# Kernel optimization log

Hardware: AMD Instinct MI355X
Metric: run time of the kernel (lower is better)

## Reference

```python
import jax, jax.numpy as jnp
import numpy as np

N = 8192; E = 131072; K = 20; IN_DIM = 3; HID = 256; N_CLASSES = 32


def setup_inputs():
    key = jax.random.key(0)
    ks = jax.random.split(key, 16)

    def w(k, shape):
        lim = 1.0 / np.sqrt(shape[0])
        return jax.random.uniform(k, shape, jnp.float32, -lim, lim)

    f32 = jnp.float32
    return {
        "features": jax.random.normal(ks[0], (N, IN_DIM), f32),
        "src": jax.random.randint(ks[1], (E,), 0, N, jnp.int32),
        "dst": jax.random.randint(ks[2], (E,), 0, N, jnp.int32),
        # GraphConv params
        "Wc1": w(ks[3], (IN_DIM, HID)), "bc1": jnp.zeros((HID,), f32),
        "Wc2": w(ks[4], (HID, HID)), "bc2": jnp.zeros((HID,), f32),
        "Wc3": w(ks[5], (64, N_CLASSES)), "bc3": jnp.zeros((N_CLASSES,), f32),
        # DynamicEdgeConv 1 MLP: [2*256 -> 256 -> 256], Linear+BN+ReLU each
        "W11": w(ks[6], (2 * HID, 256)), "b11": jnp.zeros((256,), f32), "g11": jnp.ones((256,), f32), "be11": jnp.zeros((256,), f32),
        "W12": w(ks[7], (256, 256)), "b12": jnp.zeros((256,), f32), "g12": jnp.ones((256,), f32), "be12": jnp.zeros((256,), f32),
        # DynamicEdgeConv 2 MLP: [2*256 -> 64 -> 64]
        "W21": w(ks[8], (2 * 256, 64)), "b21": jnp.zeros((64,), f32), "g21": jnp.ones((64,), f32), "be21": jnp.zeros((64,), f32),
        "W22": w(ks[9], (64, 64)), "b22": jnp.zeros((64,), f32), "g22": jnp.ones((64,), f32), "be22": jnp.zeros((64,), f32),
    }


def reference(features, src, dst, Wc1, bc1, Wc2, bc2, Wc3, bc3,
              W11, b11, g11, be11, W12, b12, g12, be12,
              W21, b21, g21, be21, W22, b22, g22, be22):
    n = features.shape[0]
    ones_e = jnp.ones(src.shape[0], features.dtype)
    # DGL GraphConv norm='both': deg clamped to min 1
    dout = jnp.clip(jax.ops.segment_sum(ones_e, src, num_segments=n), 1.0) ** -0.5
    din = jnp.clip(jax.ops.segment_sum(ones_e, dst, num_segments=n), 1.0) ** -0.5

    def gconv(x, W, b, act):
        agg = jax.ops.segment_sum((x * dout[:, None])[src], dst, num_segments=n)
        r = (agg * din[:, None]) @ W + b
        return jax.nn.relu(r) if act else r

    def bn(x, g, b):  # BatchNorm1d in training mode over all edge rows
        mu = jnp.mean(x, axis=(0, 1), keepdims=True)
        var = jnp.mean(jnp.square(x - mu), axis=(0, 1), keepdims=True)
        return (x - mu) * jax.lax.rsqrt(var + 1e-5) * g + b

    def edge_conv(x, layers):
        # dynamic kNN graph on current features (self included, dist 0)
        sq = jnp.sum(x * x, axis=-1)
        d = sq[:, None] + sq[None, :] - 2.0 * (x @ x.T)  # [N,N]
        idx = jax.lax.top_k(-d, K)[1]                    # [N,K]
        xi = x[:, None, :]
        e = jnp.concatenate([jnp.broadcast_to(xi, (n, K, x.shape[-1])), x[idx] - xi], axis=-1)  # [N,K,2F]
        for W, b, g, be in layers:
            e = jax.nn.relu(bn(e @ W + b, g, be))
        return jnp.max(e, axis=1)  # max aggregation over neighbors

    h = gconv(features, Wc1, bc1, True)                                   # [N,256]
    h = edge_conv(h, [(W11, b11, g11, be11), (W12, b12, g12, be12)])      # [N,256]
    h = gconv(h, Wc2, bc2, True)                                          # [N,256]
    h = edge_conv(h, [(W21, b21, g21, be21), (W22, b22, g22, be22)])      # [N,64]
    return gconv(h, Wc3, bc3, False)                                      # [N,32]
```

## Files before the change

kernel.cpp:

```cpp
#include <hip/hip_runtime.h>

#define NN 8192
#define NE 131072
#define KNN 20
#define CH 4096
#define GBM 128
#define GBN 128
#define GBK 64

typedef __attribute__((ext_vector_type(4))) float f32x4;
typedef __attribute__((ext_vector_type(8))) __bf16 bf16x8;

__global__ void k_zero(float* p, int n){
  int i = blockIdx.x*256 + threadIdx.x;
  if (i < n) p[i] = 0.f;
}
__global__ void k_zero_i(int* p, int n){
  int i = blockIdx.x*256 + threadIdx.x;
  if (i < n) p[i] = 0;
}

__device__ __forceinline__ unsigned short f2bf(float x){
  unsigned u = __float_as_uint(x);
  unsigned r = (u + 0x7fff + ((u >> 16) & 1)) >> 16;
  return (unsigned short)r;
}
__device__ __forceinline__ float bf2f(unsigned short h){
  return __uint_as_float((unsigned)h << 16);
}
__device__ __forceinline__ void gload16(const void* g, void* l){
  __builtin_amdgcn_global_load_lds(
      (const __attribute__((address_space(1))) void*)g,
      (__attribute__((address_space(3))) void*)l, 16, 0, 0);
}

__global__ void k_count(const int* __restrict__ src, const int* __restrict__ dst,
                        int* cs, int* cd){
  int e = blockIdx.x*256 + threadIdx.x;
  if (e < NE){ atomicAdd(&cs[src[e]], 1); atomicAdd(&cd[dst[e]], 1); }
}
__global__ void k_deg(const int* cs, const int* cd, float* dout, float* din){
  int i = blockIdx.x*256 + threadIdx.x;
  if (i < NN){
    dout[i] = rsqrtf((float)max(cs[i], 1));
    din[i]  = rsqrtf((float)max(cd[i], 1));
  }
}
__global__ void k_scan(const int* __restrict__ cnt, int* __restrict__ off){
  __shared__ int sh[256];
  __shared__ int carry;
  int tid = threadIdx.x;
  if (tid == 0) carry = 0;
  __syncthreads();
  for (int base = 0; base < NN; base += 256){
    int v = cnt[base + tid];
    int x = v;
    sh[tid] = x; __syncthreads();
    for (int o = 1; o < 256; o <<= 1){
      int y = (tid >= o) ? sh[tid - o] : 0;
      __syncthreads();
      x += y; sh[tid] = x;
      __syncthreads();
    }
    off[base + tid] = carry + x - v;
    __syncthreads();
    if (tid == 255){
      carry += x;
      if (base + 256 == NN) off[NN] = carry;
    }
    __syncthreads();
  }
}
__global__ void k_fill(const int* __restrict__ src, const int* __restrict__ dst,
                       const int* __restrict__ roff, int* cursor, int* csr){
  int e = blockIdx.x*256 + threadIdx.x;
  if (e < NE){
    int d = dst[e];
    int p = atomicAdd(&cursor[d], 1);
    csr[roff[d] + p] = src[e];
  }
}

__global__ void k_gconv1(const float* __restrict__ feat, const int* __restrict__ roff,
                         const int* __restrict__ csr, const float* __restrict__ dout,
                         const float* __restrict__ din, const float* __restrict__ Wc1,
                         const float* __restrict__ bc1, float* __restrict__ h1){
  int wid = threadIdx.x >> 6, lane = threadIdx.x & 63;
  int i = blockIdx.x*4 + wid;
  float a0=0.f, a1=0.f, a2=0.f;
  int beg = roff[i], end = roff[i+1];
  for (int t = beg + lane; t < end; t += 64){
    int s = csr[t]; float w = dout[s];
    a0 += feat[s*3+0]*w; a1 += feat[s*3+1]*w; a2 += feat[s*3+2]*w;
  }
  for (int m = 32; m; m >>= 1){
    a0 += __shfl_xor(a0, m); a1 += __shfl_xor(a1, m); a2 += __shfl_xor(a2, m);
  }
  float dn = din[i];
  a0 *= dn; a1 *= dn; a2 *= dn;
  for (int c = lane; c < 256; c += 64){
    float r = a0*Wc1[c] + a1*Wc1[256+c] + a2*Wc1[512+c] + bc1[c];
    h1[(size_t)i*256 + c] = fmaxf(r, 0.f);
  }
}

__global__ void k_sq(const float* __restrict__ X, float* __restrict__ sq){
  int wid = threadIdx.x >> 6, lane = threadIdx.x & 63;
  int i = blockIdx.x*4 + wid;
  float4 v = *(const float4*)&X[(size_t)i*256 + lane*4];
  float s = v.x*v.x + v.y*v.y + v.z*v.z + v.w*v.w;
  for (int m = 32; m; m >>= 1) s += __shfl_xor(s, m);
  if (lane == 0) sq[i] = s;
}

__global__ void k_split(const float* __restrict__ X, unsigned short* __restrict__ xcat){
  int row = blockIdx.x, c = threadIdx.x;
  float x = X[(size_t)row*256 + c];
  unsigned short h = f2bf(x);
  unsigned short lo = f2bf(x - bf2f(h));
  xcat[(size_t)row*512 + c] = h;
  xcat[(size_t)row*512 + 256 + c] = lo;
}

__global__ void k_wsplit(const float* __restrict__ W, unsigned short* __restrict__ Whi,
                         unsigned short* __restrict__ Wlo){
  int k = blockIdx.x, n = threadIdx.x;
  float x = W[(size_t)k*256 + n];
  unsigned short h = f2bf(x);
  Whi[(size_t)n*256 + k] = h;
  Wlo[(size_t)n*256 + k] = f2bf(x - bf2f(h));
}
__global__ void k_wsplit64(const float* __restrict__ W, unsigned short* __restrict__ Whi,
                           unsigned short* __restrict__ Wlo){
  int k = blockIdx.x, n = threadIdx.x;
  float x = W[(size_t)k*64 + n];
  unsigned short h = f2bf(x);
  Whi[(size_t)n*64 + k] = h;
  Wlo[(size_t)n*64 + k] = f2bf(x - bf2f(h));
}

__global__ __launch_bounds__(256)
void k_gram_mfma(const unsigned short* __restrict__ Xcat,
                 float* __restrict__ G, int r0){
  __shared__ unsigned short sA[GBM*GBK];
  __shared__ unsigned short sB[GBM*GBK];
  int tid = threadIdx.x;
  int lw = tid >> 6, l = tid & 63;
  int rbl = blockIdx.y*GBM;
  int rb = r0 + rbl;
  int cb = blockIdx.x*GBN;

  int srow = l >> 3;
  int scol = (l & 7) ^ srow;
  const unsigned short* srcA[4];
  const unsigned short* srcB[4];
  char* dstA[4]; char* dstB[4];
  #pragma unroll
  for (int i = 0; i < 4; i++){
    int c = lw*4 + i;
    int row = c*8 + srow;
    srcA[i] = Xcat + (size_t)(rb + row)*512 + scol*8;
    srcB[i] = Xcat + (size_t)(cb + row)*512 + scol*8;
    dstA[i] = (char*)sA + c*1024;
    dstB[i] = (char*)sB + c*1024;
  }

  int wm = lw >> 1, wn = lw & 1;
  int fm = l & 15, kg = l >> 4;
  unsigned offA[4][2], offB[4][2];
  #pragma unroll
  for (int mf = 0; mf < 4; mf++){
    int rowa = wm*64 + mf*16 + fm;
    int rowb = wn*64 + mf*16 + fm;
    #pragma unroll
    for (int ks = 0; ks < 2; ks++){
      offA[mf][ks] = rowa*128 + (((unsigned)(ks*4 + kg) ^ (rowa & 7)))*16;
      offB[mf][ks] = rowb*128 + (((unsigned)(ks*4 + kg) ^ (rowb & 7)))*16;
    }
  }

  f32x4 acc[4][4];
  #pragma unroll
  for (int m = 0; m < 4; m++)
    #pragma unroll
    for (int n = 0; n < 4; n++) acc[m][n] = (f32x4){0.f,0.f,0.f,0.f};

  #pragma unroll
  for (int s = 0; s < 12; s++){
    int sec = s >> 2;
    int inner = (s & 3)*64;
    int cbA = (sec == 1 ? 256 : 0) + inner;
    int cbB = (sec == 2 ? 256 : 0) + inner;
    #pragma unroll
    for (int i = 0; i < 4; i++){
      gload16(srcA[i] + cbA, dstA[i]);
      gload16(srcB[i] + cbB, dstB[i]);
    }
    __syncthreads();
    #pragma unroll
    for (int ks = 0; ks < 2; ks++){
      bf16x8 a[4], b[4];
      #pragma unroll
      for (int mf = 0; mf < 4; mf++) a[mf] = *(const bf16x8*)((const char*)sA + offA[mf][ks]);
      #pragma unroll
      for (int nf = 0; nf < 4; nf++) b[nf] = *(const bf16x8*)((const char*)sB + offB[nf][ks]);
      #pragma unroll
      for (int mf = 0; mf < 4; mf++)
        #pragma unroll
        for (int nf = 0; nf < 4; nf++)
          acc[mf][nf] = __builtin_amdgcn_mfma_f32_16x16x32_bf16(a[mf], b[nf], acc[mf][nf], 0, 0, 0);
    }
    __syncthreads();
  }

  #pragma unroll
  for (int mf = 0; mf < 4; mf++){
    int orow = rbl + wm*64 + mf*16 + kg*4;
    #pragma unroll
    for (int nf = 0; nf < 4; nf++){
      int ocol = cb + wn*64 + nf*16 + fm;
      #pragma unroll
      for (int r = 0; r < 4; r++)
        G[(size_t)(orow + r)*NN + ocol] = acc[mf][nf][r];
    }
  }
}

__global__ __launch_bounds__(256)
void k_topk(const float* __restrict__ G, const float* __restrict__ sq,
            int r0, int* __restrict__ idxo){
  __shared__ float lsq[NN];
  int tid = threadIdx.x;
  for (int t = tid; t < NN/4; t += 256)
    ((float4*)lsq)[t] = ((const float4*)sq)[t];
  __syncthreads();

  int wid = tid >> 6, lane = tid & 63;
  int rl = blockIdx.x*4 + wid;
  int gr = r0 + rl;
  const float4* row4 = (const float4*)(G + (size_t)rl*NN);
  const float4* lsq4 = (const float4*)lsq;
  float sqr = lsq[gr];

  float kd0=INFINITY,kd1=INFINITY,kd2=INFINITY,kd3=INFINITY,kd4=INFINITY,
        kd5=INFINITY,kd6=INFINITY,kd7=INFINITY,kd8=INFINITY,kd9=INFINITY,
        kd10=INFINITY,kd11=INFINITY,kd12=INFINITY,kd13=INFINITY,kd14=INFINITY,
        kd15=INFINITY,kd16=INFINITY,kd17=INFINITY,kd18=INFINITY,kd19=INFINITY;
  int ki0=0x7fffffff,ki1=0x7fffffff,ki2=0x7fffffff,ki3=0x7fffffff,ki4=0x7fffffff,
      ki5=0x7fffffff,ki6=0x7fffffff,ki7=0x7fffffff,ki8=0x7fffffff,ki9=0x7fffffff,
      ki10=0x7fffffff,ki11=0x7fffffff,ki12=0x7fffffff,ki13=0x7fffffff,ki14=0x7fffffff,
      ki15=0x7fffffff,ki16=0x7fffffff,ki17=0x7fffffff,ki18=0x7fffffff,ki19=0x7fffffff;

#define ST(U) { bool sw = nk < kd##U; float tv = kd##U; int tq = ki##U; \
      if (sw){ kd##U = nk; ki##U = ni; nk = tv; ni = tq; } }
#define INSE(kc, jc) { if ((kc) < kd19){ float nk = (kc); int ni = (jc); \
      ST(0) ST(1) ST(2) ST(3) ST(4) ST(5) ST(6) ST(7) ST(8) ST(9) \
      ST(10) ST(11) ST(12) ST(13) ST(14) ST(15) ST(16) ST(17) ST(18) ST(19) } }

  float4 gc = row4[lane];
  float4 sc = lsq4[lane];
  #pragma unroll 1
  for (int o = 0; o < 32; o++){
    float4 g = gc, s = sc;
    if (o < 31){
      gc = row4[lane + (o+1)*64];
      sc = lsq4[lane + (o+1)*64];
    }
    int jb = (lane + o*64)*4;
    float k0 = (sqr + s.x) - 2.f*g.x;
    float k1 = (sqr + s.y) - 2.f*g.y;
    float k2 = (sqr + s.z) - 2.f*g.z;
    float k3 = (sqr + s.w) - 2.f*g.w;
    float t19 = kd19;
    float mn = fminf(fminf(k0,k1), fminf(k2,k3));
    if (__any(mn < t19)){
      INSE(k0, jb+0);
      INSE(k1, jb+1);
      INSE(k2, jb+2);
      INSE(k3, jb+3);
    }
  }
#undef INSE
#undef ST

#define MV(A,B) { kd##A = kd##B; ki##A = ki##B; }
  #pragma unroll 1
  for (int r = 0; r < KNN; r++){
    float bv = kd0; int bi = ki0;
    #pragma unroll
    for (int mm = 32; mm; mm >>= 1){
      float ov = __shfl_xor(bv, mm); int oi = __shfl_xor(bi, mm);
      if (ov < bv || (ov == bv && oi < bi)){ bv = ov; bi = oi; }
    }
    if (ki0 == bi){
      MV(0,1) MV(1,2) MV(2,3) MV(3,4) MV(4,5) MV(5,6) MV(6,7) MV(7,8) MV(8,9) MV(9,10)
      MV(10,11) MV(11,12) MV(12,13) MV(13,14) MV(14,15) MV(15,16) MV(16,17) MV(17,18) MV(18,19)
      kd19 = INFINITY; ki19 = 0x7fffffff;
    }
    if (lane == 0) idxo[(size_t)gr*KNN + r] = bi;
  }
#undef MV
}

__global__ void k_wd(const float* __restrict__ W, float* __restrict__ Wd, int rows, int M){
  int t = blockIdx.x*256 + threadIdx.x;
  if (t < rows*M) Wd[t] = W[t] - W[rows*M + t];
}

__global__ __launch_bounds__(256)
void k_mm(const float* __restrict__ A, const float* __restrict__ B,
          const float* __restrict__ bias, float* __restrict__ Cout,
          int n, int Kd, int M, int relu){
  __shared__ float la[16][68], lb[16][68];
  int tid = threadIdx.x;
  int rb = blockIdx.y*64, cb = blockIdx.x*64;
  int lr = tid >> 2, lq = (tid & 3)*4;
  int ty = tid >> 4, tx = tid & 15;
  float acc[4][4] = {};
  for (int k0 = 0; k0 < Kd; k0 += 16){
    __syncthreads();
    #pragma unroll
    for (int u = 0; u < 4; u++){
      int k = k0 + lq + u;
      la[lq+u][lr] = (k < Kd) ? A[(size_t)(rb+lr)*Kd + k] : 0.f;
    }
    int kk = tid >> 4; int cc = (tid & 15)*4;
    #pragma unroll
    for (int u = 0; u < 4; u++){
      int c = cb + cc + u; int k = k0 + kk;
      lb[kk][cc+u] = (k < Kd && c < M) ? B[(size_t)k*M + c] : 0.f;
    }
    __syncthreads();
    #pragma unroll
    for (int k = 0; k < 16; k++){
      float4 a = *(const float4*)&la[k][ty*4];
      float4 b = *(const float4*)&lb[k][tx*4];
      float avv[4] = {a.x,a.y,a.z,a.w}, bvv[4] = {b.x,b.y,b.z,b.w};
      #pragma unroll
      for (int u = 0; u < 4; u++)
        #pragma unroll
        for (int v = 0; v < 4; v++) acc[u][v] += avv[u]*bvv[v];
    }
  }
  #pragma unroll
  for (int u = 0; u < 4; u++){
    int r = rb + ty*4 + u;
    #pragma unroll
    for (int v = 0; v < 4; v++){
      int c = cb + tx*4 + v;
      if (c < M){
        float x = acc[u][v] + (bias ? bias[c] : 0.f);
        if (relu) x = fmaxf(x, 0.f);
        Cout[(size_t)r*M + c] = x;
      }
    }
  }
}

template<int C>
__global__ __launch_bounds__(256)
void k_stats1(const float* __restrict__ A, const float* __restrict__ P,
              const int* __restrict__ idx, float* __restrict__ ssum, float* __restrict__ ssq){
  __shared__ int si[128], sj[128];
  int tid = threadIdx.x;
  int s0 = blockIdx.x*128;
  if (tid < 128){ si[tid] = (s0 + tid)/KNN; sj[tid] = idx[s0 + tid]; }
  __syncthreads();
  constexpr int MPAR = 256/C;
  int tc = tid % C, sr = tid / C;
  float s = 0.f, q = 0.f;
  for (int m = sr; m < 128; m += MPAR){
    float v = A[(size_t)si[m]*C + tc] + P[(size_t)sj[m]*C + tc];
    s += v; q += v*v;
  }
  if constexpr (MPAR > 1){
    __shared__ float rs[256], rq[256];
    rs[tid] = s; rq[tid] = q; __syncthreads();
    if (sr == 0){
      for (int u = 1; u < MPAR; u++){ s += rs[u*C + tc]; q += rq[u*C + tc]; }
    }
  }
  if (sr == 0){ atomicAdd(&ssum[tc], s); atomicAdd(&ssq[tc], q); }
}

__global__ void k_bn_final(const float* __restrict__ ssum, const float* __restrict__ ssq,
                           const float* __restrict__ g, const float* __restrict__ be,
                           float* __restrict__ sb, float* __restrict__ tb, int C, float invn){
  int c = threadIdx.x;
  if (c < C){
    float mu = ssum[c]*invn;
    float var = fmaxf(ssq[c]*invn - mu*mu, 0.f);
    float s = g[c]*rsqrtf(var + 1e-5f);
    sb[c] = s; tb[c] = be[c] - mu*s;
  }
}

__global__ __launch_bounds__(256, 2)
void k_edge_mfma(const float* __restrict__ A, const float* __restrict__ P,
                 const int* __restrict__ idx, const float* __restrict__ sb,
                 const float* __restrict__ tb, const unsigned short* __restrict__ Wthi,
                 const unsigned short* __restrict__ Wtlo, const float* __restrict__ bias,
                 float* __restrict__ out, float* __restrict__ ssum, float* __restrict__ ssq){
  __shared__ unsigned short ehi[64*256];
  __shared__ unsigned short elo[64*256];
  __shared__ int sj[64];
  int tid = threadIdx.x;
  int lw = tid >> 6, l = tid & 63;
  int s0 = blockIdx.x*64;
  if (tid < 64) sj[tid] = idx[s0 + tid];
  float sbc = sb[tid], tbc = tb[tid];
  __syncthreads();

  #pragma unroll 1
  for (int g = 0; g < 8; g++){
    float va[8];
    #pragma unroll
    for (int u = 0; u < 8; u++){
      int it = g*8 + u;
      int i = (s0 + it)/KNN;
      int j = sj[it];
      va[u] = A[(size_t)i*256 + tid] + P[(size_t)j*256 + tid];
    }
    #pragma unroll
    for (int u = 0; u < 8; u++){
      int it = g*8 + u;
      float v = fmaxf(va[u]*sbc + tbc, 0.f);
      unsigned short h = f2bf(v);
      unsigned short lo = f2bf(v - bf2f(h));
      unsigned off = (unsigned)it*512 + (((unsigned)tid*2) ^ (((unsigned)it & 7) << 4));
      *(unsigned short*)((char*)ehi + off) = h;
      *(unsigned short*)((char*)elo + off) = lo;
    }
  }
  __syncthreads();

  int fm = l & 15, kg = l >> 4;
  const unsigned short* bhi[4];
  const unsigned short* blo[4];
  float bz[4];
  #pragma unroll
  for (int nf = 0; nf < 4; nf++){
    int col = lw*64 + nf*16 + fm;
    bhi[nf] = Wthi + (size_t)col*256 + kg*8;
    blo[nf] = Wtlo + (size_t)col*256 + kg*8;
    bz[nf] = bias[col];
  }

  f32x4 acc[4][4];
  #pragma unroll
  for (int m = 0; m < 4; m++)
    #pragma unroll
    for (int n = 0; n < 4; n++) acc[m][n] = (f32x4){0.f,0.f,0.f,0.f};

  #pragma unroll 1
  for (int sec = 0; sec < 3; sec++){
    const char* abase = (sec == 1) ? (const char*)elo : (const char*)ehi;
    int bsec = (sec == 2);
    #pragma unroll 1
    for (int st = 0; st < 8; st++){
      int g = st*4 + kg;
      bf16x8 a[4], b[4];
      #pragma unroll
      for (int mf = 0; mf < 4; mf++){
        int row = mf*16 + fm;
        a[mf] = *(const bf16x8*)(abase + row*512 + ((unsigned)(g ^ (row & 7)))*16);
      }
      #pragma unroll
      for (int nf = 0; nf < 4; nf++){
        const unsigned short* bp = bsec ? blo[nf] : bhi[nf];
        b[nf] = *(const bf16x8*)(bp + st*32);
      }
      #pragma unroll
      for (int mf = 0; mf < 4; mf++)
        #pragma unroll
        for (int nf = 0; nf < 4; nf++)
          acc[mf][nf] = __builtin_amdgcn_mfma_f32_16x16x32_bf16(a[mf], b[nf], acc[mf][nf], 0, 0, 0);
    }
  }

  float s4[4], q4[4];
  #pragma unroll
  for (int nf = 0; nf < 4; nf++){ s4[nf] = 0.f; q4[nf] = 0.f; }
  #pragma unroll
  for (int mf = 0; mf < 4; mf++){
    #pragma unroll
    for (int nf = 0; nf < 4; nf++){
      int col = lw*64 + nf*16 + fm;
      #pragma unroll
      for (int r = 0; r < 4; r++){
        int row = s0 + mf*16 + kg*4 + r;
        float v = acc[mf][nf][r] + bz[nf];
        out[(size_t)row*256 + col] = v;
        s4[nf] += v; q4[nf] += v*v;
      }
    }
  }
  #pragma unroll
  for (int nf = 0; nf < 4; nf++){
    s4[nf] += __shfl_xor(s4[nf], 16); q4[nf] += __shfl_xor(q4[nf], 16);
    s4[nf] += __shfl_xor(s4[nf], 32); q4[nf] += __shfl_xor(q4[nf], 32);
  }
  if (kg == 0){
    #pragma unroll
    for (int nf = 0; nf < 4; nf++){
      int col = lw*64 + nf*16 + fm;
      atomicAdd(&ssum[col], s4[nf]);
      atomicAdd(&ssq[col], q4[nf]);
    }
  }
}

__global__ __launch_bounds__(256, 2)
void k_edge_mfma64(const float* __restrict__ A, const float* __restrict__ P,
                   const int* __restrict__ idx, const float* __restrict__ sb,
                   const float* __restrict__ tb, const unsigned short* __restrict__ Wthi,
                   const unsigned short* __restrict__ Wtlo, const float* __restrict__ bias,
                   float* __restrict__ out, float* __restrict__ ssum, float* __restrict__ ssq){
  __shared__ unsigned short ehi[128*64];
  __shared__ unsigned short elo[128*64];
  __shared__ int sj[128];
  int tid = threadIdx.x;
  int lw = tid >> 6, l = tid & 63;
  int s0 = blockIdx.x*128;
  if (tid < 128) sj[tid] = idx[s0 + tid];
  int col0 = tid & 63, rgrp = tid >> 6;
  float sbc = sb[col0], tbc = tb[col0];
  __syncthreads();

  #pragma unroll 1
  for (int g = 0; g < 4; g++){
    float va[8];
    #pragma unroll
    for (int u = 0; u < 8; u++){
      int it = (g*8 + u)*4 + rgrp;
      int i = (s0 + it)/KNN;
      int j = sj[it];
      va[u] = A[(size_t)i*64 + col0] + P[(size_t)j*64 + col0];
    }
    #pragma unroll
    for (int u = 0; u < 8; u++){
      int it = (g*8 + u)*4 + rgrp;
      float v = fmaxf(va[u]*sbc + tbc, 0.f);
      unsigned short h = f2bf(v);
      unsigned short lo = f2bf(v - bf2f(h));
      unsigned off = (unsigned)it*128 + (((unsigned)col0*2) ^ (((unsigned)it & 7) << 4));
      *(unsigned short*)((char*)ehi + off) = h;
      *(unsigned short*)((char*)elo + off) = lo;
    }
  }
  __syncthreads();

  int wm = lw >> 1, wn = lw & 1;
  int fm = l & 15, kg = l >> 4;
  const unsigned short* bhi[2];
  const unsigned short* blo[2];
  float bz[2];
  #pragma unroll
  for (int nf = 0; nf < 2; nf++){
    int col = wn*32 + nf*16 + fm;
    bhi[nf] = Wthi + (size_t)col*64 + kg*8;
    blo[nf] = Wtlo + (size_t)col*64 + kg*8;
    bz[nf] = bias[col];
  }

  f32x4 acc[4][2];
  #pragma unroll
  for (int m = 0; m < 4; m++)
    #pragma unroll
    for (int n = 0; n < 2; n++) acc[m][n] = (f32x4){0.f,0.f,0.f,0.f};

  #pragma unroll 1
  for (int sec = 0; sec < 3; sec++){
    const char* abase = (sec == 1) ? (const char*)elo : (const char*)ehi;
    int bsec = (sec == 2);
    #pragma unroll
    for (int ks = 0; ks < 2; ks++){
      int g = ks*4 + kg;
      bf16x8 a[4], b[2];
      #pragma unroll
      for (int mf = 0; mf < 4; mf++){
        int row = wm*64 + mf*16 + fm;
        a[mf] = *(const bf16x8*)(abase + row*128 + ((unsigned)(g ^ (row & 7)))*16);
      }
      #pragma unroll
      for (int nf = 0; nf < 2; nf++){
        const unsigned short* bp = bsec ? blo[nf] : bhi[nf];
        b[nf] = *(const bf16x8*)(bp + ks*32);
      }
      #pragma unroll
      for (int mf = 0; mf < 4; mf++)
        #pragma unroll
        for (int nf = 0; nf < 2; nf++)
          acc[mf][nf] = __builtin_amdgcn_mfma_f32_16x16x32_bf16(a[mf], b[nf], acc[mf][nf], 0, 0, 0);
    }
  }

  float s2[2], q2[2];
  #pragma unroll
  for (int nf = 0; nf < 2; nf++){ s2[nf] = 0.f; q2[nf] = 0.f; }
  #pragma unroll
  for (int mf = 0; mf < 4; mf++){
    #pragma unroll
    for (int nf = 0; nf < 2; nf++){
      int col = wn*32 + nf*16 + fm;
      #pragma unroll
      for (int r = 0; r < 4; r++){
        int row = s0 + wm*64 + mf*16 + kg*4 + r;
        float v = acc[mf][nf][r] + bz[nf];
        out[(size_t)row*64 + col] = v;
        s2[nf] += v; q2[nf] += v*v;
      }
    }
  }
  #pragma unroll
  for (int nf = 0; nf < 2; nf++){
    s2[nf] += __shfl_xor(s2[nf], 16); q2[nf] += __shfl_xor(q2[nf], 16);
    s2[nf] += __shfl_xor(s2[nf], 32); q2[nf] += __shfl_xor(q2[nf], 32);
  }
  if (kg == 0){
    #pragma unroll
    for (int nf = 0; nf < 2; nf++){
      int col = wn*32 + nf*16 + fm;
      atomicAdd(&ssum[col], s2[nf]);
      atomicAdd(&ssq[col], q2[nf]);
    }
  }
}

template<int C>
__global__ void k_maxpool(const float* __restrict__ X, const float* __restrict__ sb,
                          const float* __restrict__ tb, float* __restrict__ H){
  constexpr int NPB = 256/C;
  int node = blockIdx.x*NPB + threadIdx.x / C;
  int c = threadIdx.x % C;
  float s = sb[c], t = tb[c];
  float mx = 0.f;
  for (int k = 0; k < KNN; k++){
    float v = X[(size_t)(node*KNN + k)*C + c]*s + t;
    mx = fmaxf(mx, v);
  }
  H[(size_t)node*C + c] = mx;
}

template<int C>
__global__ void k_agg(const float* __restrict__ X, const int* __restrict__ roff,
                      const int* __restrict__ csr, const float* __restrict__ dout,
                      const float* __restrict__ din, float* __restrict__ XA){
  int i = blockIdx.x; int c = threadIdx.x;
  float acc = 0.f;
  int b = roff[i], e = roff[i+1];
  for (int t = b; t < e; t++){
    int s = csr[t];
    acc += X[(size_t)s*C + c]*dout[s];
  }
  XA[(size_t)i*C + c] = acc*din[i];
}

extern "C" void kernel_launch(void* const* d_in, const int* in_sizes, int n_in,
                              void* d_out, int out_size, void* d_ws, size_t ws_size,
                              hipStream_t stream){
  const float* feat = (const float*)d_in[0];
  const int*   src  = (const int*)d_in[1];
  const int*   dst  = (const int*)d_in[2];
  const float* Wc1  = (const float*)d_in[3];
  const float* bc1  = (const float*)d_in[4];
  const float* Wc2  = (const float*)d_in[5];
  const float* bc2  = (const float*)d_in[6];
  const float* Wc3  = (const float*)d_in[7];
  const float* bc3  = (const float*)d_in[8];
  const float* W11  = (const float*)d_in[9];
  const float* b11  = (const float*)d_in[10];
  const float* g11  = (const float*)d_in[11];
  const float* be11 = (const float*)d_in[12];
  const float* W12  = (const float*)d_in[13];
  const float* b12  = (const float*)d_in[14];
  const float* g12  = (const float*)d_in[15];
  const float* be12 = (const float*)d_in[16];
  const float* W21  = (const float*)d_in[17];
  const float* b21  = (const float*)d_in[18];
  const float* g21  = (const float*)d_in[19];
  const float* be21 = (const float*)d_in[20];
  const float* W22  = (const float*)d_in[21];
  const float* b22  = (const float*)d_in[22];
  const float* g22  = (const float*)d_in[23];
  const float* be22 = (const float*)d_in[24];
  float* out = (float*)d_out;

  char* w = (char*)d_ws; size_t off = 0;
  auto alloc = [&](size_t bytes)->void*{
    void* p = w + off;
    off += bytes; off = (off + 255) & ~(size_t)255;
    return p;
  };
  int* cnt_s  = (int*)alloc(NN*4);
  int* cnt_d  = (int*)alloc(NN*4);
  int* roff   = (int*)alloc((NN+1)*4);
  int* cursor = (int*)alloc(NN*4);
  int* csr    = (int*)alloc(NE*4);
  int* idx    = (int*)alloc((size_t)NN*KNN*4);
  float* dout = (float*)alloc(NN*4);
  float* din  = (float*)alloc(NN*4);
  float* sqv  = (float*)alloc(NN*4);
  float* h1   = (float*)alloc((size_t)NN*256*4);
  float* h2   = (float*)alloc((size_t)NN*256*4);
  float* h3   = (float*)alloc((size_t)NN*256*4);
  float* h4   = (float*)alloc((size_t)NN*64*4);
  float* xa   = (float*)alloc((size_t)NN*256*4);
  float* Abuf = (float*)alloc((size_t)NN*256*4);
  float* Pbuf = (float*)alloc((size_t)NN*256*4);
  float* Wd   = (float*)alloc(256*256*4);
  float* ssum = (float*)alloc(256*4);
  float* ssq  = (float*)alloc(256*4);
  float* sbn  = (float*)alloc(256*4);
  float* tbn  = (float*)alloc(256*4);
  unsigned short* wthi = (unsigned short*)alloc(256*256*2);
  unsigned short* wtlo = (unsigned short*)alloc(256*256*2);
  unsigned short* w64hi = (unsigned short*)alloc(64*64*2);
  unsigned short* w64lo = (unsigned short*)alloc(64*64*2);
  float* out2 = (float*)alloc((size_t)NN*KNN*256*4);
  float* gram = out2;
  unsigned short* xcat = (unsigned short*)(out2 + (size_t)CH*NN);
  (void)ws_size; (void)n_in; (void)in_sizes; (void)out_size;

  const float invn = 1.0f / (float)(NN*KNN);

  k_zero_i<<<32, 256, 0, stream>>>(cnt_s, NN);
  k_zero_i<<<32, 256, 0, stream>>>(cnt_d, NN);
  k_zero_i<<<32, 256, 0, stream>>>(cursor, NN);
  k_count<<<NE/256, 256, 0, stream>>>(src, dst, cnt_s, cnt_d);
  k_deg<<<32, 256, 0, stream>>>(cnt_s, cnt_d, dout, din);
  k_scan<<<1, 256, 0, stream>>>(cnt_d, roff);
  k_fill<<<NE/256, 256, 0, stream>>>(src, dst, roff, cursor, csr);

  k_gconv1<<<NN/4, 256, 0, stream>>>(feat, roff, csr, dout, din, Wc1, bc1, h1);

  k_sq<<<NN/4, 256, 0, stream>>>(h1, sqv);
  k_split<<<NN, 256, 0, stream>>>(h1, xcat);
  for (int r0 = 0; r0 < NN; r0 += CH){
    k_gram_mfma<<<dim3(NN/GBN, CH/GBM), 256, 0, stream>>>(xcat, gram, r0);
    k_topk<<<CH/4, 256, 0, stream>>>(gram, sqv, r0, idx);
  }
  k_wd<<<256, 256, 0, stream>>>(W11, Wd, 256, 256);
  k_wsplit<<<256, 256, 0, stream>>>(W12, wthi, wtlo);
  k_mm<<<dim3(4, NN/64), 256, 0, stream>>>(h1, Wd, b11, Abuf, NN, 256, 256, 0);
  k_mm<<<dim3(4, NN/64), 256, 0, stream>>>(h1, W11 + 256*256, nullptr, Pbuf, NN, 256, 256, 0);
  k_zero<<<2, 256, 0, stream>>>(ssum, 256); k_zero<<<2, 256, 0, stream>>>(ssq, 256);
  k_stats1<256><<<NN*KNN/128, 256, 0, stream>>>(Abuf, Pbuf, idx, ssum, ssq);
  k_bn_final<<<1, 256, 0, stream>>>(ssum, ssq, g11, be11, sbn, tbn, 256, invn);
  k_zero<<<2, 256, 0, stream>>>(ssum, 256); k_zero<<<2, 256, 0, stream>>>(ssq, 256);
  k_edge_mfma<<<NN*KNN/64, 256, 0, stream>>>(Abuf, Pbuf, idx, sbn, tbn, wthi, wtlo, b12, out2, ssum, ssq);
  k_bn_final<<<1, 256, 0, stream>>>(ssum, ssq, g12, be12, sbn, tbn, 256, invn);
  k_maxpool<256><<<NN, 256, 0, stream>>>(out2, sbn, tbn, h2);

  k_agg<256><<<NN, 256, 0, stream>>>(h2, roff, csr, dout, din, xa);
  k_mm<<<dim3(4, NN/64), 256, 0, stream>>>(xa, Wc2, bc2, h3, NN, 256, 256, 1);

  k_sq<<<NN/4, 256, 0, stream>>>(h3, sqv);
  k_split<<<NN, 256, 0, stream>>>(h3, xcat);
  for (int r0 = 0; r0 < NN; r0 += CH){
    k_gram_mfma<<<dim3(NN/GBN, CH/GBM), 256, 0, stream>>>(xcat, gram, r0);
    k_topk<<<CH/4, 256, 0, stream>>>(gram, sqv, r0, idx);
  }
  k_wd<<<64, 256, 0, stream>>>(W21, Wd, 256, 64);
  k_wsplit64<<<64, 64, 0, stream>>>(W22, w64hi, w64lo);
  k_mm<<<dim3(1, NN/64), 256, 0, stream>>>(h3, Wd, b21, Abuf, NN, 256, 64, 0);
  k_mm<<<dim3(1, NN/64), 256, 0, stream>>>(h3, W21 + 256*64, nullptr, Pbuf, NN, 256, 64, 0);
  k_zero<<<2, 256, 0, stream>>>(ssum, 256); k_zero<<<2, 256, 0, stream>>>(ssq, 256);
  k_stats1<64><<<NN*KNN/128, 256, 0, stream>>>(Abuf, Pbuf, idx, ssum, ssq);
  k_bn_final<<<1, 256, 0, stream>>>(ssum, ssq, g21, be21, sbn, tbn, 64, invn);
  k_zero<<<2, 256, 0, stream>>>(ssum, 256); k_zero<<<2, 256, 0, stream>>>(ssq, 256);
  k_edge_mfma64<<<NN*KNN/128, 256, 0, stream>>>(Abuf, Pbuf, idx, sbn, tbn, w64hi, w64lo, b22, out2, ssum, ssq);
  k_bn_final<<<1, 256, 0, stream>>>(ssum, ssq, g22, be22, sbn, tbn, 64, invn);
  k_maxpool<64><<<NN/4, 256, 0, stream>>>(out2, sbn, tbn, h4);

  k_agg<64><<<NN, 64, 0, stream>>>(h4, roff, csr, dout, din, xa);
  k_mm<<<dim3(1, NN/64), 256, 0, stream>>>(xa, Wc3, bc3, out, NN, 64, 32, 0);
}
```

Before: 1.393 ms.

## Use split-bf16 MFMA for node GEMMs and shrink edge MFMA tile

Replaces the scalar fp32 tiled k_mm for the 256-wide node-level GEMMs (edge-conv layer-1 A/P projections and the GraphConv2 linear) with a new MFMA kernel. It reuses the hi/lo bf16 split activations (xcat) and split weights, using three bf16 passes to approximate fp32 accuracy. The edge MFMA kernel also halves its row tile from 64 to 32 edges per block and raises occupancy from 2 to 4 blocks. Each wave now covers 16 rows by 128 columns, trading more blocks and less A reuse for lower LDS and register use. This adds several extra weight-split and activation-split launches, and reuses xcat, which still holds the h1 split from the kNN stage.

New measurement: 1.789 ms. +28.5%, slower.

```diff
diff --git a/kernel.cpp b/kernel.cpp
--- a/kernel.cpp
+++ b/kernel.cpp
@@ -308,6 +308,61 @@
 }
 
 __global__ __launch_bounds__(256)
+void k_mm_mfma(const unsigned short* __restrict__ Xc, const unsigned short* __restrict__ Wthi,
+               const unsigned short* __restrict__ Wtlo, const float* __restrict__ bias,
+               float* __restrict__ C, int relu){
+  int tid = threadIdx.x;
+  int lw = tid >> 6, l = tid & 63;
+  int wm = lw >> 1, wn = lw & 1;
+  int fm = l & 15, kg = l >> 4;
+  int rb = blockIdx.x*32;
+
+  const unsigned short* aptr = Xc + (size_t)(rb + wm*16 + fm)*512 + kg*8;
+  const unsigned short* bhi[8];
+  const unsigned short* blo[8];
+  float bz[8];
+  #pragma unroll
+  for (int nf = 0; nf < 8; nf++){
+    int col = wn*128 + nf*16 + fm;
+    bhi[nf] = Wthi + (size_t)col*256 + kg*8;
+    blo[nf] = Wtlo + (size_t)col*256 + kg*8;
+    bz[nf] = bias ? bias[col] : 0.f;
+  }
+
+  f32x4 acc[8];
+  #pragma unroll
+  for (int n = 0; n < 8; n++) acc[n] = (f32x4){0.f,0.f,0.f,0.f};
+
+  #pragma unroll 1
+  for (int sec = 0; sec < 3; sec++){
+    int ka = (sec == 1) ? 256 : 0;
+    int bsec = (sec == 2);
+    #pragma unroll
+    for (int st = 0; st < 8; st++){
+      bf16x8 a = *(const bf16x8*)(aptr + ka + st*32);
+      #pragma unroll
+      for (int nf = 0; nf < 8; nf++){
+        const unsigned short* bp = bsec ? blo[nf] : bhi[nf];
+        bf16x8 b = *(const bf16x8*)(bp + st*32);
+        acc[nf] = __builtin_amdgcn_mfma_f32_16x16x32_bf16(a, b, acc[nf], 0, 0, 0);
+      }
+    }
+  }
+
+  #pragma unroll
+  for (int nf = 0; nf < 8; nf++){
+    int col = wn*128 + nf*16 + fm;
+    #pragma unroll
+    for (int r = 0; r < 4; r++){
+      int row = rb + wm*16 + kg*4 + r;
+      float v = acc[nf][r] + bz[nf];
+      if (relu) v = fmaxf(v, 0.f);
+      C[(size_t)row*256 + col] = v;
+    }
+  }
+}
+
+__global__ __launch_bounds__(256)
 void k_mm(const float* __restrict__ A, const float* __restrict__ B,
           const float* __restrict__ bias, float* __restrict__ Cout,
           int n, int Kd, int M, int relu){
@@ -395,24 +450,24 @@
   }
 }
 
-__global__ __launch_bounds__(256, 2)
+__global__ __launch_bounds__(256, 4)
 void k_edge_mfma(const float* __restrict__ A, const float* __restrict__ P,
                  const int* __restrict__ idx, const float* __restrict__ sb,
                  const float* __restrict__ tb, const unsigned short* __restrict__ Wthi,
                  const unsigned short* __restrict__ Wtlo, const float* __restrict__ bias,
                  float* __restrict__ out, float* __restrict__ ssum, float* __restrict__ ssq){
-  __shared__ unsigned short ehi[64*256];
-  __shared__ unsigned short elo[64*256];
-  __shared__ int sj[64];
+  __shared__ unsigned short ehi[32*256];
+  __shared__ unsigned short elo[32*256];
+  __shared__ int sj[32];
   int tid = threadIdx.x;
   int lw = tid >> 6, l = tid & 63;
-  int s0 = blockIdx.x*64;
-  if (tid < 64) sj[tid] = idx[s0 + tid];
+  int s0 = blockIdx.x*32;
+  if (tid < 32) sj[tid] = idx[s0 + tid];
   float sbc = sb[tid], tbc = tb[tid];
   __syncthreads();
 
   #pragma unroll 1
-  for (int g = 0; g < 8; g++){
+  for (int g = 0; g < 4; g++){
     float va[8];
     #pragma unroll
     for (int u = 0; u < 8; u++){
@@ -434,78 +489,58 @@
   }
   __syncthreads();
 
+  int wm = lw >> 1, wn = lw & 1;
   int fm = l & 15, kg = l >> 4;
-  const unsigned short* bhi[4];
-  const unsigned short* blo[4];
-  float bz[4];
-  #pragma unroll
-  for (int nf = 0; nf < 4; nf++){
-    int col = lw*64 + nf*16 + fm;
+  const unsigned short* bhi[8];
+  const unsigned short* blo[8];
+  float bz[8];
+  #pragma unroll
+  for (int nf = 0; nf < 8; nf++){
+    int col = wn*128 + nf*16 + fm;
     bhi[nf] = Wthi + (size_t)col*256 + kg*8;
     blo[nf] = Wtlo + (size_t)col*256 + kg*8;
     bz[nf] = bias[col];
   }
 
-  f32x4 acc[4][4];
-  #pragma unroll
-  for (int m = 0; m < 4; m++)
-    #pragma unroll
-    for (int n = 0; n < 4; n++) acc[m][n] = (f32x4){0.f,0.f,0.f,0.f};
-
+  f32x4 acc[8];
+  #pragma unroll
+  for (int n = 0; n < 8; n++) acc[n] = (f32x4){0.f,0.f,0.f,0.f};
+
+  int arow = wm*16 + fm;
+  unsigned abase_off = (unsigned)arow*512;
   #pragma unroll 1
   for (int sec = 0; sec < 3; sec++){
     const char* abase = (sec == 1) ? (const char*)elo : (const char*)ehi;
     int bsec = (sec == 2);
-    #pragma unroll 1
+    #pragma unroll
     for (int st = 0; st < 8; st++){
       int g = st*4 + kg;
-      bf16x8 a[4], b[4];
-      #pragma unroll
-      for (int mf = 0; mf < 4; mf++){
-        int row = mf*16 + fm;
-        a[mf] = *(const bf16x8*)(abase + row*512 + ((unsigned)(g ^ (row & 7)))*16);
+      bf16x8 a = *(const bf16x8*)(abase + abase_off + ((unsigned)(g ^ (arow & 7)))*16);
+      #pragma unroll
+      for (int nf = 0; nf < 8; nf++){
+        const unsigned short* bp = bsec ? blo[nf] : bhi[nf];
+        bf16x8 b = *(const bf16x8*)(bp + st*32);
+        acc[nf] = __builtin_amdgcn_mfma_f32_16x16x32_bf16(a, b, acc[nf], 0, 0, 0);
       }
-      #pragma unroll
-      for (int nf = 0; nf < 4; nf++){
-        const unsigned short* bp = bsec ? blo[nf] : bhi[nf];
-        b[nf] = *(const bf16x8*)(bp + st*32);
-      }
-      #pragma unroll
-      for (int mf = 0; mf < 4; mf++)
-        #pragma unroll
-        for (int nf = 0; nf < 4; nf++)
-          acc[mf][nf] = __builtin_amdgcn_mfma_f32_16x16x32_bf16(a[mf], b[nf], acc[mf][nf], 0, 0, 0);
-    }
-  }
-
-  float s4[4], q4[4];
-  #pragma unroll
-  for (int nf = 0; nf < 4; nf++){ s4[nf] = 0.f; q4[nf] = 0.f; }
-  #pragma unroll
-  for (int mf = 0; mf < 4; mf++){
-    #pragma unroll
-    for (int nf = 0; nf < 4; nf++){
-      int col = lw*64 + nf*16 + fm;
-      #pragma unroll
-      for (int r = 0; r < 4; r++){
-        int row = s0 + mf*16 + kg*4 + r;
-        float v = acc[mf][nf][r] + bz[nf];
-        out[(size_t)row*256 + col] = v;
-        s4[nf] += v; q4[nf] += v*v;
-      }
-    }
-  }
-  #pragma unroll
-  for (int nf = 0; nf < 4; nf++){
-    s4[nf] += __shfl_xor(s4[nf], 16); q4[nf] += __shfl_xor(q4[nf], 16);
-    s4[nf] += __shfl_xor(s4[nf], 32); q4[nf] += __shfl_xor(q4[nf], 32);
-  }
-  if (kg == 0){
-    #pragma unroll
-    for (int nf = 0; nf < 4; nf++){
-      int col = lw*64 + nf*16 + fm;
-      atomicAdd(&ssum[col], s4[nf]);
-      atomicAdd(&ssq[col], q4[nf]);
+    }
+  }
+
+  #pragma unroll
+  for (int nf = 0; nf < 8; nf++){
+    int col = wn*128 + nf*16 + fm;
+    float s4 = 0.f, q4 = 0.f;
+    #pragma unroll
+    for (int r = 0; r < 4; r++){
+      int row = s0 + wm*16 + kg*4 + r;
+      float v = acc[nf][r] + bz[nf];
+      out[(size_t)row*256 + col] = v;
+      s4 += v; q4 += v*v;
+    }
+    s4 += __shfl_xor(s4, 16); q4 += __shfl_xor(q4, 16);
+    s4 += __shfl_xor(s4, 32); q4 += __shfl_xor(q4, 32);
+    if (kg == 0){
+      atomicAdd(&ssum[col], s4);
+      atomicAdd(&ssq[col], q4);
     }
   }
 }
@@ -715,6 +750,12 @@
   float* tbn  = (float*)alloc(256*4);
   unsigned short* wthi = (unsigned short*)alloc(256*256*2);
   unsigned short* wtlo = (unsigned short*)alloc(256*256*2);
+  unsigned short* wdhi = (unsigned short*)alloc(256*256*2);
+  unsigned short* wdlo = (unsigned short*)alloc(256*256*2);
+  unsigned short* wbhi = (unsigned short*)alloc(256*256*2);
+  unsigned short* wblo = (unsigned short*)alloc(256*256*2);
+  unsigned short* wchi = (unsigned short*)alloc(256*256*2);
+  unsigned short* wclo = (unsigned short*)alloc(256*256*2);
   unsigned short* w64hi = (unsigned short*)alloc(64*64*2);
   unsigned short* w64lo = (unsigned short*)alloc(64*64*2);
   float* out2 = (float*)alloc((size_t)NN*KNN*256*4);
@@ -741,19 +782,23 @@
     k_topk<<<CH/4, 256, 0, stream>>>(gram, sqv, r0, idx);
   }
   k_wd<<<256, 256, 0, stream>>>(W11, Wd, 256, 256);
+  k_wsplit<<<256, 256, 0, stream>>>(Wd, wdhi, wdlo);
+  k_wsplit<<<256, 256, 0, stream>>>(W11 + 256*256, wbhi, wblo);
   k_wsplit<<<256, 256, 0, stream>>>(W12, wthi, wtlo);
-  k_mm<<<dim3(4, NN/64), 256, 0, stream>>>(h1, Wd, b11, Abuf, NN, 256, 256, 0);
-  k_mm<<<dim3(4, NN/64), 256, 0, stream>>>(h1, W11 + 256*256, nullptr, Pbuf, NN, 256, 256, 0);
+  k_mm_mfma<<<NN/32, 256, 0, stream>>>(xcat, wdhi, wdlo, b11, Abuf, 0);
+  k_mm_mfma<<<NN/32, 256, 0, stream>>>(xcat, wbhi, wblo, nullptr, Pbuf, 0);
   k_zero<<<2, 256, 0, stream>>>(ssum, 256); k_zero<<<2, 256, 0, stream>>>(ssq, 256);
   k_stats1<256><<<NN*KNN/128, 256, 0, stream>>>(Abuf, Pbuf, idx, ssum, ssq);
   k_bn_final<<<1, 256, 0, stream>>>(ssum, ssq, g11, be11, sbn, tbn, 256, invn);
   k_zero<<<2, 256, 0, stream>>>(ssum, 256); k_zero<<<2, 256, 0, stream>>>(ssq, 256);
-  k_edge_mfma<<<NN*KNN/64, 256, 0, stream>>>(Abuf, Pbuf, idx, sbn, tbn, wthi, wtlo, b12, out2, ssum, ssq);
+  k_edge_mfma<<<NN*KNN/32, 256, 0, stream>>>(Abuf, Pbuf, idx, sbn, tbn, wthi, wtlo, b12, out2, ssum, ssq);
   k_bn_final<<<1, 256, 0, stream>>>(ssum, ssq, g12, be12, sbn, tbn, 256, invn);
   k_maxpool<256><<<NN, 256, 0, stream>>>(out2, sbn, tbn, h2);
 
   k_agg<256><<<NN, 256, 0, stream>>>(h2, roff, csr, dout, din, xa);
-  k_mm<<<dim3(4, NN/64), 256, 0, stream>>>(xa, Wc2, bc2, h3, NN, 256, 256, 1);
+  k_split<<<NN, 256, 0, stream>>>(xa, xcat);
+  k_wsplit<<<256, 256, 0, stream>>>(Wc2, wchi, wclo);
+  k_mm_mfma<<<NN/32, 256, 0, stream>>>(xcat, wchi, wclo, bc2, h3, 1);
 
   k_sq<<<NN/4, 256, 0, stream>>>(h3, sqv);
   k_split<<<NN, 256, 0, stream>>>(h3, xcat);
```

## Fuse distance epilogue into gram kernel and move 256-wide linears to MFMA

Applied to the files above, without the earlier changes.

The gram kernel now loads squared norms into shared memory and writes full squared distances, so the top-k kernel no longer stages an 8192-entry norm table per block or does the per-element distance arithmetic. The three 256x256 dense matmuls (the two edge-conv1 projections and the GraphConv2 linear) move from the scalar fp32 k_mm to a new bf16 MFMA kernel. That kernel uses a hi/lo split of activations and weights to keep close to fp32 accuracy. This adds extra split kernels for weights and activations, and the three-term split drops the lo*lo product, which may slightly change kNN selection.

Result: no change. 1.397 ms (median of 2 runs) (+0.3%).

```diff
diff --git a/kernel.cpp b/kernel.cpp
--- a/kernel.cpp
+++ b/kernel.cpp
@@ -140,15 +140,20 @@
 }
 
 __global__ __launch_bounds__(256)
-void k_gram_mfma(const unsigned short* __restrict__ Xcat,
+void k_gram_mfma(const unsigned short* __restrict__ Xcat, const float* __restrict__ sq,
                  float* __restrict__ G, int r0){
   __shared__ unsigned short sA[GBM*GBK];
   __shared__ unsigned short sB[GBM*GBK];
+  __shared__ float sqr[GBM];
+  __shared__ float sqc[GBN];
   int tid = threadIdx.x;
   int lw = tid >> 6, l = tid & 63;
   int rbl = blockIdx.y*GBM;
   int rb = r0 + rbl;
   int cb = blockIdx.x*GBN;
+
+  if (tid < GBM) sqr[tid] = sq[rb + tid];
+  else if (tid < GBM + GBN) sqc[tid - GBM] = sq[cb + tid - GBM];
 
   int srow = l >> 3;
   int scol = (l & 7) ^ srow;
@@ -215,32 +220,25 @@
 
   #pragma unroll
   for (int mf = 0; mf < 4; mf++){
-    int orow = rbl + wm*64 + mf*16 + kg*4;
+    int lr0 = wm*64 + mf*16 + kg*4;
     #pragma unroll
     for (int nf = 0; nf < 4; nf++){
-      int ocol = cb + wn*64 + nf*16 + fm;
+      int lc = wn*64 + nf*16 + fm;
+      float sc = sqc[lc];
       #pragma unroll
       for (int r = 0; r < 4; r++)
-        G[(size_t)(orow + r)*NN + ocol] = acc[mf][nf][r];
+        G[(size_t)(rbl + lr0 + r)*NN + cb + lc] = (sqr[lr0 + r] + sc) - 2.f*acc[mf][nf][r];
     }
   }
 }
 
 __global__ __launch_bounds__(256)
-void k_topk(const float* __restrict__ G, const float* __restrict__ sq,
-            int r0, int* __restrict__ idxo){
-  __shared__ float lsq[NN];
+void k_topk(const float* __restrict__ G, int r0, int* __restrict__ idxo){
   int tid = threadIdx.x;
-  for (int t = tid; t < NN/4; t += 256)
-    ((float4*)lsq)[t] = ((const float4*)sq)[t];
-  __syncthreads();
-
   int wid = tid >> 6, lane = tid & 63;
   int rl = blockIdx.x*4 + wid;
   int gr = r0 + rl;
   const float4* row4 = (const float4*)(G + (size_t)rl*NN);
-  const float4* lsq4 = (const float4*)lsq;
-  float sqr = lsq[gr];
 
   float kd0=INFINITY,kd1=INFINITY,kd2=INFINITY,kd3=INFINITY,kd4=INFINITY,
         kd5=INFINITY,kd6=INFINITY,kd7=INFINITY,kd8=INFINITY,kd9=INFINITY,
@@ -258,26 +256,18 @@
       ST(10) ST(11) ST(12) ST(13) ST(14) ST(15) ST(16) ST(17) ST(18) ST(19) } }
 
   float4 gc = row4[lane];
-  float4 sc = lsq4[lane];
   #pragma unroll 1
   for (int o = 0; o < 32; o++){
-    float4 g = gc, s = sc;
-    if (o < 31){
-      gc = row4[lane + (o+1)*64];
-      sc = lsq4[lane + (o+1)*64];
-    }
+    float4 g = gc;
+    if (o < 31) gc = row4[lane + (o+1)*64];
     int jb = (lane + o*64)*4;
-    float k0 = (sqr + s.x) - 2.f*g.x;
-    float k1 = (sqr + s.y) - 2.f*g.y;
-    float k2 = (sqr + s.z) - 2.f*g.z;
-    float k3 = (sqr + s.w) - 2.f*g.w;
     float t19 = kd19;
-    float mn = fminf(fminf(k0,k1), fminf(k2,k3));
+    float mn = fminf(fminf(g.x, g.y), fminf(g.z, g.w));
     if (__any(mn < t19)){
-      INSE(k0, jb+0);
-      INSE(k1, jb+1);
-      INSE(k2, jb+2);
-      INSE(k3, jb+3);
+      INSE(g.x, jb+0);
+      INSE(g.y, jb+1);
+      INSE(g.z, jb+2);
+      INSE(g.w, jb+3);
     }
   }
 #undef INSE
@@ -305,6 +295,61 @@
 __global__ void k_wd(const float* __restrict__ W, float* __restrict__ Wd, int rows, int M){
   int t = blockIdx.x*256 + threadIdx.x;
   if (t < rows*M) Wd[t] = W[t] - W[rows*M + t];
+}
+
+__global__ __launch_bounds__(256)
+void k_mm_mfma(const unsigned short* __restrict__ Xc, const unsigned short* __restrict__ Wthi,
+               const unsigned short* __restrict__ Wtlo, const float* __restrict__ bias,
+               float* __restrict__ C, int relu){
+  int tid = threadIdx.x;
+  int lw = tid >> 6, l = tid & 63;
+  int wm = lw >> 1, wn = lw & 1;
+  int fm = l & 15, kg = l >> 4;
+  int rb = blockIdx.x*32;
+
+  const unsigned short* aptr = Xc + (size_t)(rb + wm*16 + fm)*512 + kg*8;
+  const unsigned short* bhi[8];
+  const unsigned short* blo[8];
+  float bz[8];
+  #pragma unroll
+  for (int nf = 0; nf < 8; nf++){
+    int col = wn*128 + nf*16 + fm;
+    bhi[nf] = Wthi + (size_t)col*256 + kg*8;
+    blo[nf] = Wtlo + (size_t)col*256 + kg*8;
+    bz[nf] = bias ? bias[col] : 0.f;
+  }
+
+  f32x4 acc[8];
+  #pragma unroll
+  for (int n = 0; n < 8; n++) acc[n] = (f32x4){0.f,0.f,0.f,0.f};
+
+  #pragma unroll 1
+  for (int sec = 0; sec < 3; sec++){
+    int ka = (sec == 1) ? 256 : 0;
+    int bsec = (sec == 2);
+    #pragma unroll
+    for (int st = 0; st < 8; st++){
+      bf16x8 a = *(const bf16x8*)(aptr + ka + st*32);
+      #pragma unroll
+      for (int nf = 0; nf < 8; nf++){
+        const unsigned short* bp = bsec ? blo[nf] : bhi[nf];
+        bf16x8 b = *(const bf16x8*)(bp + st*32);
+        acc[nf] = __builtin_amdgcn_mfma_f32_16x16x32_bf16(a, b, acc[nf], 0, 0, 0);
+      }
+    }
+  }
+
+  #pragma unroll
+  for (int nf = 0; nf < 8; nf++){
+    int col = wn*128 + nf*16 + fm;
+    #pragma unroll
+    for (int r = 0; r < 4; r++){
+      int row = rb + wm*16 + kg*4 + r;
+      float v = acc[nf][r] + bz[nf];
+      if (relu) v = fmaxf(v, 0.f);
+      C[(size_t)row*256 + col] = v;
+    }
+  }
 }
 
 __global__ __launch_bounds__(256)
@@ -715,6 +760,12 @@
   float* tbn  = (float*)alloc(256*4);
   unsigned short* wthi = (unsigned short*)alloc(256*256*2);
   unsigned short* wtlo = (unsigned short*)alloc(256*256*2);
+  unsigned short* wdhi = (unsigned short*)alloc(256*256*2);
+  unsigned short* wdlo = (unsigned short*)alloc(256*256*2);
+  unsigned short* wbhi = (unsigned short*)alloc(256*256*2);
+  unsigned short* wblo = (unsigned short*)alloc(256*256*2);
+  unsigned short* wchi = (unsigned short*)alloc(256*256*2);
+  unsigned short* wclo = (unsigned short*)alloc(256*256*2);
   unsigned short* w64hi = (unsigned short*)alloc(64*64*2);
   unsigned short* w64lo = (unsigned short*)alloc(64*64*2);
   float* out2 = (float*)alloc((size_t)NN*KNN*256*4);
@@ -737,13 +788,15 @@
   k_sq<<<NN/4, 256, 0, stream>>>(h1, sqv);
   k_split<<<NN, 256, 0, stream>>>(h1, xcat);
   for (int r0 = 0; r0 < NN; r0 += CH){
-    k_gram_mfma<<<dim3(NN/GBN, CH/GBM), 256, 0, stream>>>(xcat, gram, r0);
-    k_topk<<<CH/4, 256, 0, stream>>>(gram, sqv, r0, idx);
+    k_gram_mfma<<<dim3(NN/GBN, CH/GBM), 256, 0, stream>>>(xcat, sqv, gram, r0);
+    k_topk<<<CH/4, 256, 0, stream>>>(gram, r0, idx);
   }
   k_wd<<<256, 256, 0, stream>>>(W11, Wd, 256, 256);
+  k_wsplit<<<256, 256, 0, stream>>>(Wd, wdhi, wdlo);
+  k_wsplit<<<256, 256, 0, stream>>>(W11 + 256*256, wbhi, wblo);
   k_wsplit<<<256, 256, 0, stream>>>(W12, wthi, wtlo);
-  k_mm<<<dim3(4, NN/64), 256, 0, stream>>>(h1, Wd, b11, Abuf, NN, 256, 256, 0);
-  k_mm<<<dim3(4, NN/64), 256, 0, stream>>>(h1, W11 + 256*256, nullptr, Pbuf, NN, 256, 256, 0);
+  k_mm_mfma<<<NN/32, 256, 0, stream>>>(xcat, wdhi, wdlo, b11, Abuf, 0);
+  k_mm_mfma<<<NN/32, 256, 0, stream>>>(xcat, wbhi, wblo, nullptr, Pbuf, 0);
   k_zero<<<2, 256, 0, stream>>>(ssum, 256); k_zero<<<2, 256, 0, stream>>>(ssq, 256);
   k_stats1<256><<<NN*KNN/128, 256, 0, stream>>>(Abuf, Pbuf, idx, ssum, ssq);
   k_bn_final<<<1, 256, 0, stream>>>(ssum, ssq, g11, be11, sbn, tbn, 256, invn);
@@ -753,13 +806,15 @@
   k_maxpool<256><<<NN, 256, 0, stream>>>(out2, sbn, tbn, h2);
 
   k_agg<256><<<NN, 256, 0, stream>>>(h2, roff, csr, dout, din, xa);
-  k_mm<<<dim3(4, NN/64), 256, 0, stream>>>(xa, Wc2, bc2, h3, NN, 256, 256, 1);
+  k_split<<<NN, 256, 0, stream>>>(xa, xcat);
+  k_wsplit<<<256, 256, 0, stream>>>(Wc2, wchi, wclo);
+  k_mm_mfma<<<NN/32, 256, 0, stream>>>(xcat, wchi, wclo, bc2, h3, 1);
 
   k_sq<<<NN/4, 256, 0, stream>>>(h3, sqv);
   k_split<<<NN, 256, 0, stream>>>(h3, xcat);
   for (int r0 = 0; r0 < NN; r0 += CH){
-    k_gram_mfma<<<dim3(NN/GBN, CH/GBM), 256, 0, stream>>>(xcat, gram, r0);
-    k_topk<<<CH/4, 256, 0, stream>>>(gram, sqv, r0, idx);
+    k_gram_mfma<<<dim3(NN/GBN, CH/GBM), 256, 0, stream>>>(xcat, sqv, gram, r0);
+    k_topk<<<CH/4, 256, 0, stream>>>(gram, r0, idx);
   }
   k_wd<<<64, 256, 0, stream>>>(W21, Wd, 256, 64);
   k_wsplit64<<<64, 64, 0, stream>>>(W22, w64hi, w64lo);
```
